# Kernel tuning notes

Measured on AMD Instinct MI355X. Metric: run time of the kernel, lower is better.

The kernel has to match this reference:

```python
import jax, jax.numpy as jnp
import numpy as np
from jax import lax

B_, T_, C_ = 8, 1024, 768
H_, W_ = 32, 32
N_LAYER, LAYER_ID = 12, 5


def _fancy_init():
    # faithful 'fancy' init from Random_SpatialMix._init_weights
    r01 = LAYER_ID / (N_LAYER - 1)
    r1a0 = 1.0 - LAYER_ID / N_LAYER
    h = np.arange(C_, dtype=np.float64)
    decay = -5 + 8 * (h / (C_ - 1)) ** (0.7 + 1.3 * r01)
    zig = ((np.arange(C_) + 1) % 3 - 1) * 0.5
    first = np.log(0.3) + zig
    xlin = h / C_
    mix_k = xlin ** r1a0
    mix_v = xlin ** r1a0 + 0.3 * r01
    mix_r = xlin ** (0.5 * r1a0)
    f32 = lambda a: jnp.asarray(a, jnp.float32)
    return f32(decay), f32(first), f32(mix_k), f32(mix_v), f32(mix_r)


def setup_inputs() -> dict:
    key = jax.random.key(0)
    ks = jax.random.split(key, 6)
    s = 1.0 / np.sqrt(C_)
    x = jax.random.normal(ks[0], (B_, T_, C_), jnp.float32)
    Wk = jax.random.normal(ks[1], (C_, C_), jnp.float32) * s
    Wv = jax.random.normal(ks[2], (C_, C_), jnp.float32) * s
    Wr = jax.random.normal(ks[3], (C_, C_), jnp.float32) * s
    Wo = jax.random.normal(ks[4], (C_, C_), jnp.float32) * s
    decay, first, mk, mv, mr = _fancy_init()
    perm = jax.random.permutation(ks[5], C_).astype(jnp.int32)
    return dict(x=x, w_key=Wk, w_value=Wv, w_receptance=Wr, w_output=Wo,
                spatial_decay=decay, spatial_first=first,
                mix_k=mk, mix_v=mv, mix_r=mr, perm=perm, H=H_, W=W_)


def _shift2d(a, dh, dw, H, W):
    # zero-padded 2D shift of [B,H,W,g]
    pad = [(0, 0), (max(dh, 0), max(-dh, 0)), (max(dw, 0), max(-dw, 0)), (0, 0)]
    a = jnp.pad(a, pad)
    return a[:, max(-dh, 0):max(-dh, 0) + H, max(-dw, 0):max(-dw, 0) + W, :]


def q_shift(x, H, W, shift_pixel=1, gamma=0.25):
    # VRWKV q_shift: 4 channel groups shifted right/left/down/up, rest copied
    B, T, C = x.shape
    xi = x.reshape(B, H, W, C)
    g = int(C * gamma)
    parts = [
        _shift2d(xi[..., 0:g], 0, shift_pixel, H, W),
        _shift2d(xi[..., g:2 * g], 0, -shift_pixel, H, W),
        _shift2d(xi[..., 2 * g:3 * g], shift_pixel, 0, H, W),
        _shift2d(xi[..., 3 * g:4 * g], -shift_pixel, 0, H, W),
        xi[..., 4 * g:],
    ]
    return jnp.concatenate(parts, axis=-1).reshape(B, T, C)


def wkv(w, u, k, v):
    # RWKV-v4 WKV kernel (numerically stable form). w,u: [C]; k,v: [B,T,C]
    w = -jnp.exp(w)  # kernel applies w = -exp(w)
    B, T, C = k.shape

    def step(carry, kv):
        a, b, p = carry  # each [B,C]
        kt, vt = kv
        q = jnp.maximum(p, u + kt)
        e1 = jnp.exp(p - q)
        e2 = jnp.exp(u + kt - q)
        y = (e1 * a + e2 * vt) / (e1 * b + e2)
        q2 = jnp.maximum(p + w, kt)
        e1 = jnp.exp(p + w - q2)
        e2 = jnp.exp(kt - q2)
        return (e1 * a + e2 * vt, e1 * b + e2, q2), y

    init = (jnp.zeros((B, C), k.dtype), jnp.zeros((B, C), k.dtype),
            jnp.full((B, C), -1e38, k.dtype))
    _, y = lax.scan(step, init, (jnp.moveaxis(k, 1, 0), jnp.moveaxis(v, 1, 0)))
    return jnp.moveaxis(y, 0, 1)


def reference(x, w_key, w_value, w_receptance, w_output,
              spatial_decay, spatial_first, mix_k, mix_v, mix_r, perm, H, W):
    B, T, C = x.shape
    xx = q_shift(x, H, W)
    xk = x * mix_k + xx * (1 - mix_k)
    xv = x * mix_v + xx * (1 - mix_v)
    xr = x * mix_r + xx * (1 - mix_r)
    k = xk @ w_key.T
    v = xv @ w_value.T
    sr = jax.nn.sigmoid(xr @ w_receptance.T)
    # training path: shuffle CHANNEL axis (RevShuffle dim=2), run WKV, reverse
    ks_ = k[:, :, perm]
    vs_ = v[:, :, perm]
    wkv_s = wkv(spatial_decay / T, spatial_first / T, ks_, vs_)
    rev = jnp.zeros_like(perm).at[perm].set(jnp.arange(C, dtype=perm.dtype))
    wkv_out = wkv_s[:, :, rev]
    return (sr * wkv_out) @ w_output.T
```

## Files before the change

kernel.cpp:

```cpp
#include <hip/hip_runtime.h>
#include <hip/hip_bf16.h>
#include <stdint.h>

#define B_N 8
#define T_N 1024
#define C_N 768
#define M_N (B_N*T_N)
#define NCH 32
#define LCH (T_N/NCH)
#define BK32 32
#define KS  (C_N/BK32)

typedef __attribute__((ext_vector_type(4))) float f32x4;
typedef __attribute__((ext_vector_type(8))) short s16x8;
typedef __attribute__((ext_vector_type(4))) unsigned short u16x4;

__device__ __forceinline__ unsigned short f2bf(float f){
  unsigned int u = __float_as_uint(f);
  u += 0x7FFFu + ((u >> 16) & 1u);
  return (unsigned short)(u >> 16);
}
__device__ __forceinline__ float bf2f(unsigned short h){
  return __uint_as_float(((unsigned int)h) << 16);
}

__device__ __forceinline__ void async16(const unsigned short* g, unsigned short* l){
  __builtin_amdgcn_global_load_lds(
      (const __attribute__((address_space(1))) unsigned int*)g,
      (__attribute__((address_space(3))) unsigned int*)l, 16, 0, 0);
}

__global__ __launch_bounds__(256) void prep_mix(
    const float* __restrict__ x,
    const float* __restrict__ Wk, const float* __restrict__ Wv,
    const float* __restrict__ Wr, const float* __restrict__ Wo,
    const int* __restrict__ perm,
    const float* __restrict__ mk, const float* __restrict__ mv, const float* __restrict__ mr,
    unsigned short* __restrict__ Wall, unsigned short* __restrict__ Wop,
    unsigned short* __restrict__ xk, unsigned short* __restrict__ xv,
    unsigned short* __restrict__ xr)
{
  if (blockIdx.x < 2304){
    int idx = blockIdx.x*256 + threadIdx.x;
    int r = idx / C_N, c = idx - r*C_N;
    int pr = perm[r];
    Wall[idx]                     = f2bf(Wk[pr*C_N + c]);
    Wall[idx +   (size_t)C_N*C_N] = f2bf(Wv[pr*C_N + c]);
    Wall[idx + 2*(size_t)C_N*C_N] = f2bf(Wr[pr*C_N + c]);
    Wop[idx] = f2bf(Wo[r*C_N + perm[c]]);
    return;
  }
  int idx = (blockIdx.x - 2304)*256 + threadIdx.x;
  int n  = idx / (C_N/4);
  int c4 = (idx - n*(C_N/4)) * 4;
  int t = n & (T_N-1);
  int h = t >> 5, w = t & 31;
  int grp = c4 / 192;
  int dh = (grp==2) ? -1 : (grp==3) ? 1 : 0;
  int dw = (grp==0) ? -1 : (grp==1) ? 1 : 0;
  int h2 = h + dh, w2 = w + dw;
  bool valid = ((unsigned)h2 < 32u) && ((unsigned)w2 < 32u);
  f32x4 xc = *(const f32x4*)(x + (size_t)n*C_N + c4);
  f32x4 xx = {0.f,0.f,0.f,0.f};
  if (valid) xx = *(const f32x4*)(x + (size_t)(n + dh*32 + dw)*C_N + c4);
  f32x4 vk = *(const f32x4*)(mk + c4);
  f32x4 vv = *(const f32x4*)(mv + c4);
  f32x4 vr = *(const f32x4*)(mr + c4);
  u16x4 ok, ov, orr;
  #pragma unroll
  for (int i=0;i<4;++i){
    float d = xc[i] - xx[i];
    ok[i]  = f2bf(xx[i] + vk[i]*d);
    ov[i]  = f2bf(xx[i] + vv[i]*d);
    orr[i] = f2bf(xx[i] + vr[i]*d);
  }
  *(u16x4*)(xk + (size_t)n*C_N + c4) = ok;
  *(u16x4*)(xv + (size_t)n*C_N + c4) = ov;
  *(u16x4*)(xr + (size_t)n*C_N + c4) = orr;
}

__global__ __launch_bounds__(256, 3) void gemm_kvr(
    const unsigned short* __restrict__ xk, const unsigned short* __restrict__ xv,
    const unsigned short* __restrict__ xr,
    const unsigned short* __restrict__ Wall,
    unsigned short* __restrict__ kb, unsigned short* __restrict__ vb,
    unsigned short* __restrict__ srb)
{
  int flat = blockIdx.y * gridDim.x + blockIdx.x;
  const int xcd = flat & 7, q = flat >> 3;
  const int mb = xcd*8 + (q & 7);
  const int nb = q >> 3;
  const int m0 = mb * 128;
  const int n0 = nb * 128;
  const int z  = nb / 6;
  const unsigned short* A = (z==0)? xk : (z==1)? xv : xr;

  __shared__ union {
    struct { unsigned short As[3][128*BK32]; unsigned short Bs[3][128*BK32]; } s;
    unsigned short ct[128*132];
  } u;
  const int tid = threadIdx.x;
  const int lane = tid & 63, wid = tid >> 6;
  const int wr = wid >> 1, wc = wid & 1;
  f32x4 acc[4][4];
  #pragma unroll
  for (int i=0;i<4;++i)
    #pragma unroll
    for (int j=0;j<4;++j) acc[i][j] = (f32x4){0.f,0.f,0.f,0.f};

  const int sgcol = ((lane & 3) ^ ((lane >> 3) & 3)) * 8;
  const int srow  = lane >> 2;
  const int lr  = lane & 15;
  const int kh  = lane >> 4;
  const int phys = (kh ^ ((lr >> 1) & 3)) * 8;

  auto stage = [&](int buf, int k0){
    #pragma unroll
    for (int i=0;i<2;++i){
      int rbase = i*64 + wid*16;
      async16(&A   [(size_t)(m0 + rbase + srow)*C_N + k0 + sgcol], &u.s.As[buf][rbase*BK32]);
      async16(&Wall[(size_t)(n0 + rbase + srow)*C_N + k0 + sgcol], &u.s.Bs[buf][rbase*BK32]);
    }
  };

  auto compute = [&](int buf){
    s16x8 af[4], bfr[4];
    #pragma unroll
    for (int mi=0;mi<4;++mi) af[mi]  = *(const s16x8*)&u.s.As[buf][(wr*64 + mi*16 + lr)*BK32 + phys];
    #pragma unroll
    for (int ni=0;ni<4;++ni) bfr[ni] = *(const s16x8*)&u.s.Bs[buf][(wc*64 + ni*16 + lr)*BK32 + phys];
    __builtin_amdgcn_s_setprio(1);
    #pragma unroll
    for (int mi=0;mi<4;++mi)
      #pragma unroll
      for (int ni=0;ni<4;++ni)
        acc[mi][ni] = __builtin_amdgcn_mfma_f32_16x16x32_bf16(af[mi], bfr[ni], acc[mi][ni], 0,0,0);
    __builtin_amdgcn_s_setprio(0);
  };

  stage(0, 0);
  stage(1, BK32);
  #pragma unroll 1
  for (int t = 0; t < KS; ++t){
    if (t + 2 < KS) stage((t+2)%3, (t+2)*BK32);
    if (t + 2 < KS)      asm volatile("s_waitcnt vmcnt(8)" ::: "memory");
    else if (t + 1 < KS) asm volatile("s_waitcnt vmcnt(4)" ::: "memory");
    else                 asm volatile("s_waitcnt vmcnt(0)" ::: "memory");
    __builtin_amdgcn_s_barrier();
    compute(t%3);
    __builtin_amdgcn_s_barrier();
  }

  unsigned short* dst = (z==0)? kb : (z==1)? vb : srb;
  const int colbase = n0 - z*C_N;
  const int lr4 = (lane>>4)*4, lc = lane & 15;
  #pragma unroll
  for (int mi=0;mi<4;++mi){
    #pragma unroll
    for (int ni=0;ni<4;++ni){
      #pragma unroll
      for (int i=0;i<4;++i){
        int r  = wr*64 + mi*16 + lr4 + i;
        int cc = wc*64 + ni*16 + lc;
        float val = acc[mi][ni][i];
        if (z==2) val = 1.f/(1.f + __expf(-val));
        u.ct[r*132 + cc] = f2bf(val);
      }
    }
  }
  __builtin_amdgcn_s_barrier();
  #pragma unroll
  for (int p=0;p<8;++p){
    int f = (p*256 + tid)*8;
    int r = f >> 7, cc = f & 127;
    s16x8 v8 = *(const s16x8*)&u.ct[r*132 + cc];
    *(s16x8*)&dst[(size_t)(m0+r)*C_N + colbase + cc] = v8;
  }
}

__global__ __launch_bounds__(256, 3) void gemm_out(
    const unsigned short* __restrict__ A, const unsigned short* __restrict__ Bw,
    float* __restrict__ out)
{
  int flat = blockIdx.y * gridDim.x + blockIdx.x;
  const int xcd = flat & 7, q = flat >> 3;
  const int mb = xcd*8 + (q & 7);
  const int nb = q >> 3;
  const int m0 = mb*128, n0 = nb*128;
  __shared__ __align__(16) unsigned short As[3][128*BK32];
  __shared__ __align__(16) unsigned short Bs[3][128*BK32];
  const int tid = threadIdx.x;
  const int lane = tid & 63, wid = tid >> 6;
  const int wr = wid >> 1, wc = wid & 1;
  f32x4 acc[4][4];
  #pragma unroll
  for (int i=0;i<4;++i)
    #pragma unroll
    for (int j=0;j<4;++j) acc[i][j] = (f32x4){0.f,0.f,0.f,0.f};

  const int sgcol = ((lane & 3) ^ ((lane >> 3) & 3)) * 8;
  const int srow  = lane >> 2;
  const int lr  = lane & 15;
  const int kh  = lane >> 4;
  const int phys = (kh ^ ((lr >> 1) & 3)) * 8;

  auto stage = [&](int buf, int k0){
    #pragma unroll
    for (int i=0;i<2;++i){
      int rbase = i*64 + wid*16;
      async16(&A [(size_t)(m0 + rbase + srow)*C_N + k0 + sgcol], &As[buf][rbase*BK32]);
      async16(&Bw[(size_t)(n0 + rbase + srow)*C_N + k0 + sgcol], &Bs[buf][rbase*BK32]);
    }
  };

  auto compute = [&](int buf){
    s16x8 af[4], bfr[4];
    #pragma unroll
    for (int mi=0;mi<4;++mi) af[mi]  = *(const s16x8*)&As[buf][(wr*64 + mi*16 + lr)*BK32 + phys];
    #pragma unroll
    for (int ni=0;ni<4;++ni) bfr[ni] = *(const s16x8*)&Bs[buf][(wc*64 + ni*16 + lr)*BK32 + phys];
    __builtin_amdgcn_s_setprio(1);
    #pragma unroll
    for (int mi=0;mi<4;++mi)
      #pragma unroll
      for (int ni=0;ni<4;++ni)
        acc[mi][ni] = __builtin_amdgcn_mfma_f32_16x16x32_bf16(af[mi], bfr[ni], acc[mi][ni], 0,0,0);
    __builtin_amdgcn_s_setprio(0);
  };

  stage(0, 0);
  stage(1, BK32);
  #pragma unroll 1
  for (int t = 0; t < KS; ++t){
    if (t + 2 < KS) stage((t+2)%3, (t+2)*BK32);
    if (t + 2 < KS)      asm volatile("s_waitcnt vmcnt(8)" ::: "memory");
    else if (t + 1 < KS) asm volatile("s_waitcnt vmcnt(4)" ::: "memory");
    else                 asm volatile("s_waitcnt vmcnt(0)" ::: "memory");
    __builtin_amdgcn_s_barrier();
    compute(t%3);
    __builtin_amdgcn_s_barrier();
  }

  const int lr4 = (lane>>4)*4, lc = lane & 15;
  #pragma unroll
  for (int mi=0;mi<4;++mi)
    #pragma unroll
    for (int ni=0;ni<4;++ni)
      #pragma unroll
      for (int i=0;i<4;++i){
        int m = m0 + wr*64 + mi*16 + lr4 + i;
        int n = n0 + wc*64 + ni*16 + lc;
        out[(size_t)m*C_N + n] = acc[mi][ni][i];
      }
}

__global__ __launch_bounds__(256) void wkv_phase1(
    const unsigned short* __restrict__ kb, const unsigned short* __restrict__ vb,
    const float* __restrict__ decay,
    float* __restrict__ sa, float* __restrict__ sb, float* __restrict__ sp)
{
  int g = blockIdx.x*256 + threadIdx.x;
  int j = g % C_N;
  int cb = g / C_N;
  int b = cb % B_N, c = cb / B_N;
  float w = -__expf(decay[j] * (1.0f/T_N));
  float a = 0.f, bb = 0.f, p = -1e38f;
  size_t base = ((size_t)b*T_N + c*LCH)*C_N + j;
  #pragma unroll 4
  for (int t = 0; t < LCH; ++t){
    size_t o = base + (size_t)t*C_N;
    float kt = bf2f(kb[o]), vt = bf2f(vb[o]);
    float pw = p + w;
    float q2 = fmaxf(pw, kt);
    float e1 = __expf(pw - q2), e2 = __expf(kt - q2);
    a  = e1*a + e2*vt;
    bb = e1*bb + e2;
    p  = q2;
  }
  sa[g] = a; sb[g] = bb; sp[g] = p;
}

__global__ __launch_bounds__(256) void wkv_phase2(
    const float* __restrict__ decay,
    float* __restrict__ sa, float* __restrict__ sb, float* __restrict__ sp)
{
  int g = blockIdx.x*256 + threadIdx.x;
  int j = g % C_N, b = g / C_N;
  float w = -__expf(decay[j] * (1.0f/T_N));
  float wL = w * (float)LCH;
  float a = 0.f, bb = 0.f, p = -1e38f;
  for (int c = 0; c < NCH; ++c){
    size_t idx = ((size_t)c*B_N + b)*C_N + j;
    float la = sa[idx], lb = sb[idx], lp = sp[idx];
    sa[idx] = a; sb[idx] = bb; sp[idx] = p;
    float p1 = p + wL;
    float pn = fmaxf(p1, lp);
    float e1 = __expf(p1 - pn), e2 = __expf(lp - pn);
    a  = e1*a + e2*la;
    bb = e1*bb + e2*lb;
    p  = pn;
  }
}

__global__ __launch_bounds__(256) void wkv_phase3(
    const unsigned short* __restrict__ kb, const unsigned short* __restrict__ vb,
    const unsigned short* __restrict__ srb,
    const float* __restrict__ decay, const float* __restrict__ first,
    const float* __restrict__ sa, const float* __restrict__ sb,
    const float* __restrict__ sp,
    unsigned short* __restrict__ zp)
{
  int g = blockIdx.x*256 + threadIdx.x;
  int j = g % C_N;
  int cb = g / C_N;
  int b = cb % B_N, c = cb / B_N;
  float w = -__expf(decay[j] * (1.0f/T_N));
  float u = first[j] * (1.0f/T_N);
  float a = sa[g], bb = sb[g], p = sp[g];
  size_t base = ((size_t)b*T_N + c*LCH)*C_N + j;
  #pragma unroll 2
  for (int t = 0; t < LCH; ++t){
    size_t o = base + (size_t)t*C_N;
    float kt = bf2f(kb[o]), vt = bf2f(vb[o]);
    float uk = u + kt;
    float q  = fmaxf(p, uk);
    float e1 = __expf(p - q), e2 = __expf(uk - q);
    float y  = __fdividef(e1*a + e2*vt, e1*bb + e2);
    zp[o] = f2bf(bf2f(srb[o]) * y);
    float pw = p + w;
    float q2 = fmaxf(pw, kt);
    float e1b = __expf(pw - q2), e2b = __expf(kt - q2);
    a  = e1b*a + e2b*vt;
    bb = e1b*bb + e2b;
    p  = q2;
  }
}

extern "C" void kernel_launch(void* const* d_in, const int* in_sizes, int n_in,
                              void* d_out, int out_size, void* d_ws, size_t ws_size,
                              hipStream_t stream)
{
  const float* x     = (const float*)d_in[0];
  const float* Wk    = (const float*)d_in[1];
  const float* Wv    = (const float*)d_in[2];
  const float* Wr    = (const float*)d_in[3];
  const float* Wo    = (const float*)d_in[4];
  const float* decay = (const float*)d_in[5];
  const float* first = (const float*)d_in[6];
  const float* mk    = (const float*)d_in[7];
  const float* mv    = (const float*)d_in[8];
  const float* mr    = (const float*)d_in[9];
  const int*   perm  = (const int*)d_in[10];
  float* out = (float*)d_out;

  char* ws = (char*)d_ws;
  size_t off = 0;
  auto alloc = [&](size_t bytes)->char* {
    char* p = ws + off;
    off += (bytes + 255) & ~(size_t)255;
    return p;
  };
  const size_t MC = (size_t)M_N * C_N;
  const size_t CC = (size_t)C_N * C_N;
  const size_t SC = (size_t)NCH * B_N * C_N;
  unsigned short* xk   = (unsigned short*)alloc(MC*2);
  unsigned short* xv   = (unsigned short*)alloc(MC*2);
  unsigned short* xr   = (unsigned short*)alloc(MC*2);
  unsigned short* zp   = (unsigned short*)alloc(MC*2);
  unsigned short* Wall = (unsigned short*)alloc(CC*3*2);
  unsigned short* Wop  = (unsigned short*)alloc(CC*2);
  unsigned short* srb  = (unsigned short*)alloc(MC*2);
  unsigned short* kb   = (unsigned short*)alloc(MC*2);
  unsigned short* vb   = (unsigned short*)alloc(MC*2);
  float* sa  = (float*)alloc(SC*4);
  float* sb  = (float*)alloc(SC*4);
  float* sp  = (float*)alloc(SC*4);

  prep_mix<<<dim3(2304 + 6144), dim3(256), 0, stream>>>(
      x, Wk, Wv, Wr, Wo, perm, mk, mv, mr, Wall, Wop, xk, xv, xr);
  gemm_kvr<<<dim3(M_N/128, 3*C_N/128), dim3(256), 0, stream>>>(
      xk, xv, xr, Wall, kb, vb, srb);
  wkv_phase1<<<dim3(SC/256), dim3(256), 0, stream>>>(kb, vb, decay, sa, sb, sp);
  wkv_phase2<<<dim3(B_N*C_N/256), dim3(256), 0, stream>>>(decay, sa, sb, sp);
  wkv_phase3<<<dim3(SC/256), dim3(256), 0, stream>>>(kb, vb, srb, decay, first,
                                                     sa, sb, sp, zp);
  gemm_out<<<dim3(M_N/128, C_N/128), dim3(256), 0, stream>>>(zp, Wop, out);
}
```

Baseline: 109.7 us.

## Double-buffer GEMMs for higher occupancy and vectorize WKV scans by four channels

```diff
diff --git a/kernel.cpp b/kernel.cpp
--- a/kernel.cpp
+++ b/kernel.cpp
@@ -79,7 +79,7 @@
   *(u16x4*)(xr + (size_t)n*C_N + c4) = orr;
 }
 
-__global__ __launch_bounds__(256, 3) void gemm_kvr(
+__global__ __launch_bounds__(256, 5) void gemm_kvr(
     const unsigned short* __restrict__ xk, const unsigned short* __restrict__ xv,
     const unsigned short* __restrict__ xr,
     const unsigned short* __restrict__ Wall,
@@ -96,8 +96,8 @@
   const unsigned short* A = (z==0)? xk : (z==1)? xv : xr;
 
   __shared__ union {
-    struct { unsigned short As[3][128*BK32]; unsigned short Bs[3][128*BK32]; } s;
-    unsigned short ct[128*132];
+    struct { unsigned short As[2][128*BK32]; unsigned short Bs[2][128*BK32]; } s;
+    unsigned short ct[64*132];
   } u;
   const int tid = threadIdx.x;
   const int lane = tid & 63, wid = tid >> 6;
@@ -139,15 +139,16 @@
   };
 
   stage(0, 0);
-  stage(1, BK32);
   #pragma unroll 1
   for (int t = 0; t < KS; ++t){
-    if (t + 2 < KS) stage((t+2)%3, (t+2)*BK32);
-    if (t + 2 < KS)      asm volatile("s_waitcnt vmcnt(8)" ::: "memory");
-    else if (t + 1 < KS) asm volatile("s_waitcnt vmcnt(4)" ::: "memory");
-    else                 asm volatile("s_waitcnt vmcnt(0)" ::: "memory");
+    if (t + 1 < KS){
+      stage((t+1)&1, (t+1)*BK32);
+      asm volatile("s_waitcnt vmcnt(4)" ::: "memory");
+    } else {
+      asm volatile("s_waitcnt vmcnt(0)" ::: "memory");
+    }
     __builtin_amdgcn_s_barrier();
-    compute(t%3);
+    compute(t & 1);
     __builtin_amdgcn_s_barrier();
   }
 
@@ -155,30 +156,36 @@
   const int colbase = n0 - z*C_N;
   const int lr4 = (lane>>4)*4, lc = lane & 15;
   #pragma unroll
-  for (int mi=0;mi<4;++mi){
-    #pragma unroll
-    for (int ni=0;ni<4;++ni){
+  for (int p=0;p<2;++p){
+    if (p) __builtin_amdgcn_s_barrier();
+    if (wr == p){
       #pragma unroll
-      for (int i=0;i<4;++i){
-        int r  = wr*64 + mi*16 + lr4 + i;
-        int cc = wc*64 + ni*16 + lc;
-        float val = acc[mi][ni][i];
-        if (z==2) val = 1.f/(1.f + __expf(-val));
-        u.ct[r*132 + cc] = f2bf(val);
+      for (int mi=0;mi<4;++mi){
+        #pragma unroll
+        for (int ni=0;ni<4;++ni){
+          #pragma unroll
+          for (int i=0;i<4;++i){
+            int r  = mi*16 + lr4 + i;
+            int cc = wc*64 + ni*16 + lc;
+            float val = acc[mi][ni][i];
+            if (z==2) val = 1.f/(1.f + __expf(-val));
+            u.ct[r*132 + cc] = f2bf(val);
+          }
+        }
       }
     }
-  }
-  __builtin_amdgcn_s_barrier();
-  #pragma unroll
-  for (int p=0;p<8;++p){
-    int f = (p*256 + tid)*8;
-    int r = f >> 7, cc = f & 127;
-    s16x8 v8 = *(const s16x8*)&u.ct[r*132 + cc];
-    *(s16x8*)&dst[(size_t)(m0+r)*C_N + colbase + cc] = v8;
-  }
-}
-
-__global__ __launch_bounds__(256, 3) void gemm_out(
+    __builtin_amdgcn_s_barrier();
+    #pragma unroll
+    for (int qq=0;qq<4;++qq){
+      int f = (qq*256 + tid)*8;
+      int r = f >> 7, cc = f & 127;
+      s16x8 v8 = *(const s16x8*)&u.ct[r*132 + cc];
+      *(s16x8*)&dst[(size_t)(m0 + p*64 + r)*C_N + colbase + cc] = v8;
+    }
+  }
+}
+
+__global__ __launch_bounds__(256, 5) void gemm_out(
     const unsigned short* __restrict__ A, const unsigned short* __restrict__ Bw,
     float* __restrict__ out)
 {
@@ -187,8 +194,8 @@
   const int mb = xcd*8 + (q & 7);
   const int nb = q >> 3;
   const int m0 = mb*128, n0 = nb*128;
-  __shared__ __align__(16) unsigned short As[3][128*BK32];
-  __shared__ __align__(16) unsigned short Bs[3][128*BK32];
+  __shared__ __align__(16) unsigned short As[2][128*BK32];
+  __shared__ __align__(16) unsigned short Bs[2][128*BK32];
   const int tid = threadIdx.x;
   const int lane = tid & 63, wid = tid >> 6;
   const int wr = wid >> 1, wc = wid & 1;
@@ -229,15 +236,16 @@
   };
 
   stage(0, 0);
-  stage(1, BK32);
   #pragma unroll 1
   for (int t = 0; t < KS; ++t){
-    if (t + 2 < KS) stage((t+2)%3, (t+2)*BK32);
-    if (t + 2 < KS)      asm volatile("s_waitcnt vmcnt(8)" ::: "memory");
-    else if (t + 1 < KS) asm volatile("s_waitcnt vmcnt(4)" ::: "memory");
-    else                 asm volatile("s_waitcnt vmcnt(0)" ::: "memory");
+    if (t + 1 < KS){
+      stage((t+1)&1, (t+1)*BK32);
+      asm volatile("s_waitcnt vmcnt(4)" ::: "memory");
+    } else {
+      asm volatile("s_waitcnt vmcnt(0)" ::: "memory");
+    }
     __builtin_amdgcn_s_barrier();
-    compute(t%3);
+    compute(t & 1);
     __builtin_amdgcn_s_barrier();
   }
 
@@ -259,25 +267,38 @@
     const float* __restrict__ decay,
     float* __restrict__ sa, float* __restrict__ sb, float* __restrict__ sp)
 {
-  int g = blockIdx.x*256 + threadIdx.x;
-  int j = g % C_N;
-  int cb = g / C_N;
+  int gid = blockIdx.x*256 + threadIdx.x;
+  int jq = gid % (C_N/4);
+  int cb = gid / (C_N/4);
   int b = cb % B_N, c = cb / B_N;
-  float w = -__expf(decay[j] * (1.0f/T_N));
-  float a = 0.f, bb = 0.f, p = -1e38f;
+  int j = jq*4;
+  f32x4 dv = *(const f32x4*)(decay + j);
+  float w[4];
+  #pragma unroll
+  for (int e=0;e<4;++e) w[e] = -__expf(dv[e] * (1.0f/T_N));
+  f32x4 a = {0.f,0.f,0.f,0.f}, bbv = {0.f,0.f,0.f,0.f};
+  f32x4 p = {-1e38f,-1e38f,-1e38f,-1e38f};
   size_t base = ((size_t)b*T_N + c*LCH)*C_N + j;
-  #pragma unroll 4
+  #pragma unroll 2
   for (int t = 0; t < LCH; ++t){
     size_t o = base + (size_t)t*C_N;
-    float kt = bf2f(kb[o]), vt = bf2f(vb[o]);
-    float pw = p + w;
-    float q2 = fmaxf(pw, kt);
-    float e1 = __expf(pw - q2), e2 = __expf(kt - q2);
-    a  = e1*a + e2*vt;
-    bb = e1*bb + e2;
-    p  = q2;
-  }
-  sa[g] = a; sb[g] = bb; sp[g] = p;
+    u16x4 k4 = *(const u16x4*)(kb + o);
+    u16x4 v4 = *(const u16x4*)(vb + o);
+    #pragma unroll
+    for (int e=0;e<4;++e){
+      float kt = bf2f(k4[e]), vt = bf2f(v4[e]);
+      float pw = p[e] + w[e];
+      float q2 = fmaxf(pw, kt);
+      float e1 = __expf(pw - q2), e2 = __expf(kt - q2);
+      a[e]   = e1*a[e]   + e2*vt;
+      bbv[e] = e1*bbv[e] + e2;
+      p[e]   = q2;
+    }
+  }
+  size_t sg = (size_t)cb*C_N + j;
+  *(f32x4*)(sa + sg) = a;
+  *(f32x4*)(sb + sg) = bbv;
+  *(f32x4*)(sp + sg) = p;
 }
 
 __global__ __launch_bounds__(256) void wkv_phase2(
@@ -310,29 +331,47 @@
     const float* __restrict__ sp,
     unsigned short* __restrict__ zp)
 {
-  int g = blockIdx.x*256 + threadIdx.x;
-  int j = g % C_N;
-  int cb = g / C_N;
+  int gid = blockIdx.x*256 + threadIdx.x;
+  int jq = gid % (C_N/4);
+  int cb = gid / (C_N/4);
   int b = cb % B_N, c = cb / B_N;
-  float w = -__expf(decay[j] * (1.0f/T_N));
-  float u = first[j] * (1.0f/T_N);
-  float a = sa[g], bb = sb[g], p = sp[g];
+  int j = jq*4;
+  f32x4 dv = *(const f32x4*)(decay + j);
+  f32x4 fv = *(const f32x4*)(first + j);
+  float w[4], uu[4];
+  #pragma unroll
+  for (int e=0;e<4;++e){
+    w[e]  = -__expf(dv[e] * (1.0f/T_N));
+    uu[e] = fv[e] * (1.0f/T_N);
+  }
+  size_t sg = (size_t)cb*C_N + j;
+  f32x4 a   = *(const f32x4*)(sa + sg);
+  f32x4 bbv = *(const f32x4*)(sb + sg);
+  f32x4 p   = *(const f32x4*)(sp + sg);
   size_t base = ((size_t)b*T_N + c*LCH)*C_N + j;
   #pragma unroll 2
   for (int t = 0; t < LCH; ++t){
     size_t o = base + (size_t)t*C_N;
-    float kt = bf2f(kb[o]), vt = bf2f(vb[o]);
-    float uk = u + kt;
-    float q  = fmaxf(p, uk);
-    float e1 = __expf(p - q), e2 = __expf(uk - q);
-    float y  = __fdividef(e1*a + e2*vt, e1*bb + e2);
-    zp[o] = f2bf(bf2f(srb[o]) * y);
-    float pw = p + w;
-    float q2 = fmaxf(pw, kt);
-    float e1b = __expf(pw - q2), e2b = __expf(kt - q2);
-    a  = e1b*a + e2b*vt;
-    bb = e1b*bb + e2b;
-    p  = q2;
+    u16x4 k4 = *(const u16x4*)(kb + o);
+    u16x4 v4 = *(const u16x4*)(vb + o);
+    u16x4 s4 = *(const u16x4*)(srb + o);
+    u16x4 z4;
+    #pragma unroll
+    for (int e=0;e<4;++e){
+      float kt = bf2f(k4[e]), vt = bf2f(v4[e]);
+      float uk = uu[e] + kt;
+      float qq = fmaxf(p[e], uk);
+      float e1 = __expf(p[e] - qq), e2 = __expf(uk - qq);
+      float y  = __fdividef(e1*a[e] + e2*vt, e1*bbv[e] + e2);
+      z4[e] = f2bf(bf2f(s4[e]) * y);
+      float pw = p[e] + w[e];
+      float q2 = fmaxf(pw, kt);
+      float e1b = __expf(pw - q2), e2b = __expf(kt - q2);
+      a[e]   = e1b*a[e]   + e2b*vt;
+      bbv[e] = e1b*bbv[e] + e2b;
+      p[e]   = q2;
+    }
+    *(u16x4*)(zp + o) = z4;
   }
 }
 
@@ -380,9 +419,9 @@
       x, Wk, Wv, Wr, Wo, perm, mk, mv, mr, Wall, Wop, xk, xv, xr);
   gemm_kvr<<<dim3(M_N/128, 3*C_N/128), dim3(256), 0, stream>>>(
       xk, xv, xr, Wall, kb, vb, srb);
-  wkv_phase1<<<dim3(SC/256), dim3(256), 0, stream>>>(kb, vb, decay, sa, sb, sp);
+  wkv_phase1<<<dim3(SC/4/256), dim3(256), 0, stream>>>(kb, vb, decay, sa, sb, sp);
   wkv_phase2<<<dim3(B_N*C_N/256), dim3(256), 0, stream>>>(decay, sa, sb, sp);
-  wkv_phase3<<<dim3(SC/256), dim3(256), 0, stream>>>(kb, vb, srb, decay, first,
-                                                     sa, sb, sp, zp);
+  wkv_phase3<<<dim3(SC/4/256), dim3(256), 0, stream>>>(kb, vb, srb, decay, first,
+                                                       sa, sb, sp, zp);
   gemm_out<<<dim3(M_N/128, C_N/128), dim3(256), 0, stream>>>(zp, Wop, out);
 }
```

Result: slower. 228.7 us (+108.4%).
